# Kernel optimization log

Hardware: AMD Instinct MI355X
Metric: run time of the kernel (lower is better)

Reference implementation:

```python
import jax, jax.numpy as jnp
import numpy as np

N_NODES = 50000

def spmm(edge_row, edge_col, edge_val, x):
    # y[r] = sum_{e: row[e]==r} val[e] * x[col[e]]  (COO SpMM)
    msgs = edge_val[:, None] * x[edge_col]  # [E, F]
    return jax.ops.segment_sum(msgs, edge_row, num_segments=N_NODES)

def setup_inputs() -> dict:
    key = jax.random.key(0)
    k1, k2, k3, k4, k5, k6 = jax.random.split(key, 6)
    N, E, D_IN, D_HID, D_OUT = N_NODES, 800000, 256, 256, 128
    Y = jax.random.normal(k1, (N, D_IN), dtype=jnp.float32)
    edge_row = jax.random.randint(k2, (E,), 0, N, dtype=jnp.int32)
    edge_col = jax.random.randint(k3, (E,), 0, N, dtype=jnp.int32)
    edge_val = jax.random.uniform(k4, (E,), dtype=jnp.float32)
    stdv1 = 1.0 / np.sqrt(D_HID)
    stdv2 = 1.0 / np.sqrt(D_OUT)
    W1 = jax.random.uniform(k5, (D_IN, D_HID), minval=-stdv1, maxval=stdv1, dtype=jnp.float32)
    W2 = jax.random.uniform(k6, (D_HID, D_OUT), minval=-stdv2, maxval=stdv2, dtype=jnp.float32)
    return {"Y": Y, "edge_row": edge_row, "edge_col": edge_col,
            "edge_val": edge_val, "W1": W1, "W2": W2}

def reference(Y, edge_row, edge_col, edge_val, W1, W2):
    # GCN layer 1: dense matmul + sparse aggregation + ReLU
    h = spmm(edge_row, edge_col, edge_val, Y @ W1)
    h = jax.nn.relu(h)
    # dropout is identity in eval mode
    # GCN layer 2
    out = spmm(edge_row, edge_col, edge_val, h @ W2)
    return out
```

## Files before the change

### kernel.cpp

```cpp
#include <hip/hip_runtime.h>


#define NN 50000

typedef short s8v __attribute__((ext_vector_type(8)));
typedef float f4v __attribute__((ext_vector_type(4)));
typedef unsigned int u32;


__device__ inline unsigned int bf16_rne_bits(float x) {
    unsigned int u = __float_as_uint(x);
    return (u + 0x7FFFu + ((u >> 16) & 1u)) >> 16;
}
__device__ inline float bf16_bits_to_f32(unsigned int h) {
    return __uint_as_float(h << 16);
}
__device__ inline void split_hi_lo(float x, unsigned short& hi, unsigned short& lo) {
    unsigned int h = bf16_rne_bits(x);
    hi = (unsigned short)h;
    lo = (unsigned short)bf16_rne_bits(x - bf16_bits_to_f32(h));
}
__device__ inline void unpack2(unsigned int u, float& f0, float& f1) {
    f0 = __uint_as_float(u << 16);
    f1 = __uint_as_float(u & 0xFFFF0000u);
}

__device__ inline void gl_lds16(const void* g, void* l) {
    __builtin_amdgcn_global_load_lds(
        (const __attribute__((address_space(1))) u32*)g,
        (__attribute__((address_space(3))) u32*)l, 16, 0, 0);
}


__global__ void hist_kernel(const int* __restrict__ erow, int* __restrict__ cnt, int E) {
    int i = blockIdx.x * blockDim.x + threadIdx.x;
    int stride = gridDim.x * blockDim.x;
    for (; i < E; i += stride) atomicAdd(&cnt[erow[i]], 1);
}

#define SCAN_CHUNK 196

__global__ __launch_bounds__(256) void scan_local(const int* __restrict__ cnt,
                                                  int* __restrict__ row_ptr,
                                                  int* __restrict__ partial, int n) {
    __shared__ int lds[256];
    int t = threadIdx.x, b = blockIdx.x;
    int idx = b * SCAN_CHUNK + t;
    int v = (t < SCAN_CHUNK && idx < n) ? cnt[idx] : 0;
    lds[t] = v;
    __syncthreads();
#pragma unroll
    for (int off = 1; off < 256; off <<= 1) {
        int a = (t >= off) ? lds[t - off] : 0;
        __syncthreads();
        lds[t] += a;
        __syncthreads();
    }
    if (t < SCAN_CHUNK && idx < n) row_ptr[idx] = lds[t] - v;
    if (t == 255) partial[b] = lds[255];
}

__global__ __launch_bounds__(256) void scan_tot(int* __restrict__ partial) {
    __shared__ int lds[256];
    int t = threadIdx.x;
    int v = partial[t];
    lds[t] = v;
    __syncthreads();
#pragma unroll
    for (int off = 1; off < 256; off <<= 1) {
        int a = (t >= off) ? lds[t - off] : 0;
        __syncthreads();
        lds[t] += a;
        __syncthreads();
    }
    partial[t] = lds[t] - v;
}

__global__ __launch_bounds__(256) void scan_add(int* __restrict__ row_ptr,
                                                int* __restrict__ cursor,
                                                const int* __restrict__ partial,
                                                int n, int E) {
    int t = threadIdx.x, b = blockIdx.x;
    int idx = b * SCAN_CHUNK + t;
    if (t < SCAN_CHUNK && idx < n) {
        int rp = row_ptr[idx] + partial[b];
        row_ptr[idx] = rp;
        cursor[idx] = rp;
    }
    if (b == 0 && t == 0) row_ptr[n] = E;
}

__global__ void scatter_kernel(const int* __restrict__ erow, const int* __restrict__ ecol,
                               const float* __restrict__ eval_, int* __restrict__ cursor,
                               int2* __restrict__ meta, int E) {
    int i = blockIdx.x * blockDim.x + threadIdx.x;
    int stride = gridDim.x * blockDim.x;
    for (; i < E; i += stride) {
        int r = erow[i];
        int pos = atomicAdd(&cursor[r], 1);
        meta[pos] = make_int2(ecol[i], __float_as_int(eval_[i]));
    }
}


__global__ __launch_bounds__(256) void split_kernel(const float* __restrict__ X,
                                                    unsigned short* __restrict__ Xp, int n4) {
    int i = blockIdx.x * blockDim.x + threadIdx.x;
    int stride = gridDim.x * blockDim.x;
    for (; i < n4; i += stride) {
        float4 v = reinterpret_cast<const float4*>(X)[i];
        ushort4 h, l;
        split_hi_lo(v.x, h.x, l.x);
        split_hi_lo(v.y, h.y, l.y);
        split_hi_lo(v.z, h.z, l.z);
        split_hi_lo(v.w, h.w, l.w);
        int row = i >> 6, c4 = (i & 63) * 4;
        *reinterpret_cast<ushort4*>(Xp + (size_t)row * 512 + c4) = h;
        *reinterpret_cast<ushort4*>(Xp + (size_t)row * 512 + 256 + c4) = l;
    }
}

__global__ __launch_bounds__(256) void wsplit_kernel(const float* __restrict__ W,
                                                     unsigned short* __restrict__ Bth,
                                                     unsigned short* __restrict__ Btl,
                                                     int K, int N) {
    int idx = blockIdx.x * blockDim.x + threadIdx.x;
    if (idx >= K * N) return;
    int k = idx / N, n = idx - k * N;
    unsigned short h, l;
    split_hi_lo(W[idx], h, l);
    Bth[(size_t)n * K + k] = h;
    Btl[(size_t)n * K + k] = l;
}

__global__ __launch_bounds__(256) void gemm_tile(const unsigned short* __restrict__ Ap,
                                                 const unsigned short* __restrict__ Bth,
                                                 const unsigned short* __restrict__ Btl,
                                                 unsigned short* __restrict__ C,
                                                 int M, int N) {
    __shared__ unsigned short lds[2][12288];
    const int tid = threadIdx.x;
    const int wave = tid >> 6, lane = tid & 63;
    const int r = lane & 15, b = lane >> 4;
    const int m0 = blockIdx.x * 128, n0 = blockIdx.y * 128;
    const int wrow = (wave & 1) * 64, wcol = (wave >> 1) * 64;

    f4v acc[4][4];
#pragma unroll
    for (int mf = 0; mf < 4; ++mf)
#pragma unroll
        for (int nf = 0; nf < 4; ++nf) acc[mf][nf] = (f4v){0.f, 0.f, 0.f, 0.f};

    auto stage = [&](int buf, int s) {
        char* lb = (char*)&lds[buf][0];
#pragma unroll
        for (int c = 0; c < 2; ++c) {
            int uni = c * 4096 + wave * 1024;
            int oc = uni + lane * 16;
            int row = oc >> 6;
            int cl = ((oc >> 4) & 3) ^ ((row >> 1) & 3);
            int arow = min(m0 + row, M - 1);
            gl_lds16(Ap + (size_t)arow * 512 + s * 32 + cl * 8, lb + uni);
            int bk = (s & 7) * 32 + cl * 8;
            const size_t boff = (size_t)(n0 + row) * 256 + bk;
            gl_lds16(Bth + boff, lb + 8192 + uni);
            if (s < 8) gl_lds16(Btl + boff, lb + 16384 + uni);
        }
    };

    stage(0, 0);
    __syncthreads();

    int buf = 0;
    for (int s = 0; s < 16; ++s) {
        if (s < 15) stage(buf ^ 1, s + 1);

        const char* lb = (const char*)&lds[buf][0];
        s8v af[4], bh[4], bl[4];
#pragma unroll
        for (int mf = 0; mf < 4; ++mf) {
            int trow = wrow + mf * 16 + r;
            int cp = b ^ ((trow >> 1) & 3);
            af[mf] = *reinterpret_cast<const s8v*>(lb + trow * 64 + cp * 16);
        }
#pragma unroll
        for (int nf = 0; nf < 4; ++nf) {
            int trow = wcol + nf * 16 + r;
            int cp = b ^ ((trow >> 1) & 3);
            bh[nf] = *reinterpret_cast<const s8v*>(lb + 8192 + trow * 64 + cp * 16);
            if (s < 8)
                bl[nf] = *reinterpret_cast<const s8v*>(lb + 16384 + trow * 64 + cp * 16);
        }
#pragma unroll
        for (int mf = 0; mf < 4; ++mf)
#pragma unroll
            for (int nf = 0; nf < 4; ++nf)
                acc[mf][nf] = __builtin_amdgcn_mfma_f32_16x16x32_bf16(af[mf], bh[nf], acc[mf][nf], 0, 0, 0);
        if (s < 8) {
#pragma unroll
            for (int mf = 0; mf < 4; ++mf)
#pragma unroll
                for (int nf = 0; nf < 4; ++nf)
                    acc[mf][nf] = __builtin_amdgcn_mfma_f32_16x16x32_bf16(af[mf], bl[nf], acc[mf][nf], 0, 0, 0);
        }
        __syncthreads();
        buf ^= 1;
    }

#pragma unroll
    for (int mf = 0; mf < 4; ++mf)
#pragma unroll
        for (int i = 0; i < 4; ++i) {
            int grow = m0 + wrow + mf * 16 + b * 4 + i;
            if (grow < M) {
#pragma unroll
                for (int nf = 0; nf < 4; ++nf)
                    C[(size_t)grow * N + n0 + wcol + nf * 16 + r] =
                        (unsigned short)bf16_rne_bits(acc[mf][nf][i]);
            }
        }
}


template <int D, bool SPLITOUT>
__global__ __launch_bounds__(256) void spmm_bf16(const int* __restrict__ row_ptr,
                                                 const int2* __restrict__ meta,
                                                 const unsigned short* __restrict__ Xb,
                                                 float* __restrict__ Yo,
                                                 unsigned short* __restrict__ Ysplit,
                                                 int nrows) {
    constexpr int VEC = D / 64;
    const int lane = threadIdx.x & 63;
    const int wid = __builtin_amdgcn_readfirstlane(threadIdx.x >> 6);
    const int r = blockIdx.x * 4 + wid;
    if (r >= nrows) return;
    const int s = row_ptr[r];
    const int e = row_ptr[r + 1];
    const unsigned short* __restrict__ base = Xb + (size_t)lane * VEC;

    float acc[VEC];
#pragma unroll
    for (int k = 0; k < VEC; ++k) acc[k] = 0.f;

    int i = s;
    for (; i + 8 <= e; i += 8) {
        int2 mm[8];
#pragma unroll
        for (int u = 0; u < 8; ++u) mm[u] = meta[i + u];
        float xv[8][VEC];
#pragma unroll
        for (int u = 0; u < 8; ++u) {
            const unsigned short* p = base + (size_t)mm[u].x * D;
            if constexpr (VEC == 4) {
                uint2 t = *reinterpret_cast<const uint2*>(p);
                unpack2(t.x, xv[u][0], xv[u][1]);
                unpack2(t.y, xv[u][2], xv[u][3]);
            } else {
                unsigned int t = *reinterpret_cast<const unsigned int*>(p);
                unpack2(t, xv[u][0], xv[u][1]);
            }
        }
#pragma unroll
        for (int u = 0; u < 8; ++u) {
            float v = __int_as_float(mm[u].y);
#pragma unroll
            for (int k = 0; k < VEC; ++k) acc[k] = fmaf(v, xv[u][k], acc[k]);
        }
    }
    for (; i < e; ++i) {
        int2 m = meta[i];
        const unsigned short* p = base + (size_t)m.x * D;
        float xv[VEC];
        if constexpr (VEC == 4) {
            uint2 t = *reinterpret_cast<const uint2*>(p);
            unpack2(t.x, xv[0], xv[1]);
            unpack2(t.y, xv[2], xv[3]);
        } else {
            unsigned int t = *reinterpret_cast<const unsigned int*>(p);
            unpack2(t, xv[0], xv[1]);
        }
        float v = __int_as_float(m.y);
#pragma unroll
        for (int k = 0; k < VEC; ++k) acc[k] = fmaf(v, xv[k], acc[k]);
    }

    if constexpr (SPLITOUT) {
        static_assert(VEC == 4, "split path assumes D=256");
        ushort4 h, l;
        float a0 = fmaxf(acc[0], 0.f), a1 = fmaxf(acc[1], 0.f);
        float a2 = fmaxf(acc[2], 0.f), a3 = fmaxf(acc[3], 0.f);
        split_hi_lo(a0, h.x, l.x);
        split_hi_lo(a1, h.y, l.y);
        split_hi_lo(a2, h.z, l.z);
        split_hi_lo(a3, h.w, l.w);
        reinterpret_cast<ushort4*>(Ysplit + (size_t)r * 512)[lane] = h;
        reinterpret_cast<ushort4*>(Ysplit + (size_t)r * 512 + 256)[lane] = l;
    } else {
        float* yp = Yo + (size_t)r * D + lane * VEC;
        if constexpr (VEC == 4) {
            *reinterpret_cast<float4*>(yp) = make_float4(acc[0], acc[1], acc[2], acc[3]);
        } else {
            *reinterpret_cast<float2*>(yp) = make_float2(acc[0], acc[1]);
        }
    }
}


extern "C" void kernel_launch(void* const* d_in, const int* in_sizes, int n_in,
                              void* d_out, int out_size, void* d_ws, size_t ws_size,
                              hipStream_t stream) {
    const float* Y     = (const float*)d_in[0];
    const int*   erow  = (const int*)d_in[1];
    const int*   ecol  = (const int*)d_in[2];
    const float* eval_ = (const float*)d_in[3];
    const float* W1    = (const float*)d_in[4];
    const float* W2    = (const float*)d_in[5];
    float* out = (float*)d_out;
    const int E = in_sizes[1];
    const int N = NN;

    char* ws = (char*)d_ws;
    unsigned short* Yp = (unsigned short*)ws;
    unsigned short* Hb = (unsigned short*)(ws + 51200000);
    char* p = ws + 76800000;
    unsigned short* B1th = (unsigned short*)p; p += 131072;
    unsigned short* B1tl = (unsigned short*)p; p += 131072;
    unsigned short* B2th = (unsigned short*)p; p += 65536;
    unsigned short* B2tl = (unsigned short*)p; p += 65536;
    int* row_ptr = (int*)p; p += 200064;
    int* cursor  = (int*)p; p += 200000;
    int* cnt     = (int*)p; p += 200000;
    int* partial = (int*)p; p += 1024;
    int2* meta   = (int2*)p;

    hipMemsetAsync(cnt, 0, (size_t)N * 4, stream);
    hist_kernel<<<512, 256, 0, stream>>>(erow, cnt, E);
    scan_local<<<256, 256, 0, stream>>>(cnt, row_ptr, partial, N);
    scan_tot<<<1, 256, 0, stream>>>(partial);
    scan_add<<<256, 256, 0, stream>>>(row_ptr, cursor, partial, N, E);
    scatter_kernel<<<512, 256, 0, stream>>>(erow, ecol, eval_, cursor, meta, E);

    split_kernel<<<2048, 256, 0, stream>>>(Y, Yp, N * 64);
    wsplit_kernel<<<256, 256, 0, stream>>>(W1, B1th, B1tl, 256, 256);
    wsplit_kernel<<<128, 256, 0, stream>>>(W2, B2th, B2tl, 256, 128);

    gemm_tile<<<dim3(391, 2), 256, 0, stream>>>(Yp, B1th, B1tl, Hb, N, 256);
    spmm_bf16<256, true><<<(N + 3) / 4, 256, 0, stream>>>(row_ptr, meta, Hb, nullptr, Yp, N);

    gemm_tile<<<dim3(391, 1), 256, 0, stream>>>(Yp, B2th, B2tl, Hb, N, 128);
    spmm_bf16<128, false><<<(N + 3) / 4, 256, 0, stream>>>(row_ptr, meta, Hb, out, nullptr, N);
}
```

Baseline: 362.1 us.

## Build CSR via two-level bucket sort with LDS atomics instead of global atomics

Replaces the global-atomic histogram, three-kernel scan and global-atomic scatter with a two-pass bucket sort. Edges are first binned into 256 row buckets using per-block LDS histograms and a single-block scan, then each bucket is sorted locally in LDS to produce row_ptr and meta. This aims to remove contended global atomics and the memset, at the cost of an extra pass through intermediate brow/bcv buffers and a serial single-block scan over 200K counters.

```diff
diff --git a/kernel.cpp b/kernel.cpp
--- a/kernel.cpp
+++ b/kernel.cpp
@@ -2,6 +2,9 @@
 
 
 #define NN 50000
+#define NBUCKET 256
+#define RPB 196
+#define PBLK 782
 
 typedef short s8v __attribute__((ext_vector_type(8)));
 typedef float f4v __attribute__((ext_vector_type(4)));
@@ -32,73 +35,106 @@
 }
 
 
-__global__ void hist_kernel(const int* __restrict__ erow, int* __restrict__ cnt, int E) {
-    int i = blockIdx.x * blockDim.x + threadIdx.x;
-    int stride = gridDim.x * blockDim.x;
-    for (; i < E; i += stride) atomicAdd(&cnt[erow[i]], 1);
-}
-
-#define SCAN_CHUNK 196
-
-__global__ __launch_bounds__(256) void scan_local(const int* __restrict__ cnt,
-                                                  int* __restrict__ row_ptr,
-                                                  int* __restrict__ partial, int n) {
-    __shared__ int lds[256];
-    int t = threadIdx.x, b = blockIdx.x;
-    int idx = b * SCAN_CHUNK + t;
-    int v = (t < SCAN_CHUNK && idx < n) ? cnt[idx] : 0;
-    lds[t] = v;
-    __syncthreads();
-#pragma unroll
+__global__ __launch_bounds__(256) void bucket_hist(const int* __restrict__ erow,
+                                                   int* __restrict__ cnt2d, int E) {
+    __shared__ int h[NBUCKET];
+    const int t = threadIdx.x, blk = blockIdx.x;
+    h[t] = 0;
+    __syncthreads();
+#pragma unroll
+    for (int u = 0; u < 4; ++u) {
+        int i = blk * 1024 + u * 256 + t;
+        if (i < E) atomicAdd(&h[erow[i] / RPB], 1);
+    }
+    __syncthreads();
+    cnt2d[t * PBLK + blk] = h[t];
+}
+
+__global__ __launch_bounds__(1024) void bucket_scan(int* __restrict__ cnt2d,
+                                                    int* __restrict__ bucket_base,
+                                                    int* __restrict__ row_ptr,
+                                                    int n, int E) {
+    __shared__ int lds[1024];
+    const int TOT = NBUCKET * PBLK;
+    const int t = threadIdx.x;
+    const int chunk = (TOT + 1023) / 1024;
+    int lo = t * chunk, hi = min(TOT, lo + chunk);
+    int s = 0;
+    for (int i = lo; i < hi; ++i) s += cnt2d[i];
+    lds[t] = s;
+    __syncthreads();
+    for (int off = 1; off < 1024; off <<= 1) {
+        int v = (t >= off) ? lds[t - off] : 0;
+        __syncthreads();
+        lds[t] += v;
+        __syncthreads();
+    }
+    int run = lds[t] - s;
+    for (int i = lo; i < hi; ++i) {
+        int c = cnt2d[i];
+        cnt2d[i] = run;
+        run += c;
+    }
+    __syncthreads();
+    if (t < NBUCKET) bucket_base[t] = cnt2d[t * PBLK];
+    if (t == 0) {
+        bucket_base[NBUCKET] = E;
+        row_ptr[n] = E;
+    }
+}
+
+__global__ __launch_bounds__(256) void bucket_scatter(const int* __restrict__ erow,
+                                                      const int* __restrict__ ecol,
+                                                      const float* __restrict__ eval_,
+                                                      const int* __restrict__ base2d,
+                                                      int* __restrict__ brow,
+                                                      int2* __restrict__ bcv, int E) {
+    __shared__ int cur[NBUCKET];
+    const int t = threadIdx.x, blk = blockIdx.x;
+    cur[t] = base2d[t * PBLK + blk];
+    __syncthreads();
+#pragma unroll
+    for (int u = 0; u < 4; ++u) {
+        int i = blk * 1024 + u * 256 + t;
+        if (i < E) {
+            int r = erow[i];
+            int pos = atomicAdd(&cur[r / RPB], 1);
+            brow[pos] = r;
+            bcv[pos] = make_int2(ecol[i], __float_as_int(eval_[i]));
+        }
+    }
+}
+
+__global__ __launch_bounds__(256) void bucket_build(const int* __restrict__ brow,
+                                                    const int2* __restrict__ bcv,
+                                                    const int* __restrict__ bucket_base,
+                                                    int* __restrict__ row_ptr,
+                                                    int2* __restrict__ meta, int n) {
+    __shared__ int h[256];
+    __shared__ int cur[256];
+    const int t = threadIdx.x, b = blockIdx.x;
+    const int s = bucket_base[b];
+    const int e = bucket_base[b + 1];
+    const int row0 = b * RPB;
+    h[t] = 0;
+    __syncthreads();
+    for (int i = s + t; i < e; i += 256) atomicAdd(&h[brow[i] - row0], 1);
+    __syncthreads();
+    int v = h[t];
     for (int off = 1; off < 256; off <<= 1) {
-        int a = (t >= off) ? lds[t - off] : 0;
-        __syncthreads();
-        lds[t] += a;
-        __syncthreads();
-    }
-    if (t < SCAN_CHUNK && idx < n) row_ptr[idx] = lds[t] - v;
-    if (t == 255) partial[b] = lds[255];
-}
-
-__global__ __launch_bounds__(256) void scan_tot(int* __restrict__ partial) {
-    __shared__ int lds[256];
-    int t = threadIdx.x;
-    int v = partial[t];
-    lds[t] = v;
-    __syncthreads();
-#pragma unroll
-    for (int off = 1; off < 256; off <<= 1) {
-        int a = (t >= off) ? lds[t - off] : 0;
-        __syncthreads();
-        lds[t] += a;
-        __syncthreads();
-    }
-    partial[t] = lds[t] - v;
-}
-
-__global__ __launch_bounds__(256) void scan_add(int* __restrict__ row_ptr,
-                                                int* __restrict__ cursor,
-                                                const int* __restrict__ partial,
-                                                int n, int E) {
-    int t = threadIdx.x, b = blockIdx.x;
-    int idx = b * SCAN_CHUNK + t;
-    if (t < SCAN_CHUNK && idx < n) {
-        int rp = row_ptr[idx] + partial[b];
-        row_ptr[idx] = rp;
-        cursor[idx] = rp;
-    }
-    if (b == 0 && t == 0) row_ptr[n] = E;
-}
-
-__global__ void scatter_kernel(const int* __restrict__ erow, const int* __restrict__ ecol,
-                               const float* __restrict__ eval_, int* __restrict__ cursor,
-                               int2* __restrict__ meta, int E) {
-    int i = blockIdx.x * blockDim.x + threadIdx.x;
-    int stride = gridDim.x * blockDim.x;
-    for (; i < E; i += stride) {
-        int r = erow[i];
-        int pos = atomicAdd(&cursor[r], 1);
-        meta[pos] = make_int2(ecol[i], __float_as_int(eval_[i]));
+        int a = (t >= off) ? h[t - off] : 0;
+        __syncthreads();
+        h[t] += a;
+        __syncthreads();
+    }
+    int rp = s + h[t] - v;
+    int grow = row0 + t;
+    if (t < RPB && grow < n) row_ptr[grow] = rp;
+    cur[t] = rp;
+    __syncthreads();
+    for (int i = s + t; i < e; i += 256) {
+        int pos = atomicAdd(&cur[brow[i] - row0], 1);
+        meta[pos] = bcv[i];
     }
 }
 
@@ -327,18 +363,17 @@
     unsigned short* B1tl = (unsigned short*)p; p += 131072;
     unsigned short* B2th = (unsigned short*)p; p += 65536;
     unsigned short* B2tl = (unsigned short*)p; p += 65536;
-    int* row_ptr = (int*)p; p += 200064;
-    int* cursor  = (int*)p; p += 200000;
-    int* cnt     = (int*)p; p += 200000;
-    int* partial = (int*)p; p += 1024;
-    int2* meta   = (int2*)p;
-
-    hipMemsetAsync(cnt, 0, (size_t)N * 4, stream);
-    hist_kernel<<<512, 256, 0, stream>>>(erow, cnt, E);
-    scan_local<<<256, 256, 0, stream>>>(cnt, row_ptr, partial, N);
-    scan_tot<<<1, 256, 0, stream>>>(partial);
-    scan_add<<<256, 256, 0, stream>>>(row_ptr, cursor, partial, N, E);
-    scatter_kernel<<<512, 256, 0, stream>>>(erow, ecol, eval_, cursor, meta, E);
+    int* row_ptr     = (int*)p; p += 200064;
+    int* cnt2d       = (int*)p; p += NBUCKET * PBLK * 4;
+    int* bucket_base = (int*)p; p += 1088;
+    int* brow        = (int*)p; p += 3200000;
+    int2* bcv        = (int2*)p; p += 6400000;
+    int2* meta       = (int2*)p;
+
+    bucket_hist<<<PBLK, 256, 0, stream>>>(erow, cnt2d, E);
+    bucket_scan<<<1, 1024, 0, stream>>>(cnt2d, bucket_base, row_ptr, N, E);
+    bucket_scatter<<<PBLK, 256, 0, stream>>>(erow, ecol, eval_, cnt2d, brow, bcv, E);
+    bucket_build<<<NBUCKET, 256, 0, stream>>>(brow, bcv, bucket_base, row_ptr, meta, N);
 
     split_kernel<<<2048, 256, 0, stream>>>(Y, Yp, N * 64);
     wsplit_kernel<<<256, 256, 0, stream>>>(W1, B1th, B1tl, 256, 256);
```

After: 604.3 us. 1.67x slower.
